# Kernel optimization log

Measured on AMD Instinct MI355X. Metric: run time of the kernel, lower is better.

The kernel has to match this reference:

```python
import jax, jax.numpy as jnp
import numpy as np

EMBED_DIM = 1024
NUM_HEADS = 16
HEAD_DIM = EMBED_DIM // NUM_HEADS
SEG_LENS = [2048, 2048, 4096]
DIL_RATES = [1, 2, 4]
SCALE = 1.0 / np.sqrt(HEAD_DIM)


def _hilbert_perm(L):
    """1D permutation ordering indices of a length-L segment along a Hilbert curve
    on the smallest 2^k x 2^k grid with >= L cells (row-major linearization)."""
    n = 1
    while n * n < L:
        n *= 2
    d = np.arange(n * n)
    x = np.zeros_like(d)
    y = np.zeros_like(d)
    t = d.copy()
    s = 1
    while s < n:
        rx = 1 & (t // 2)
        ry = 1 & (t ^ rx)
        swap = ry == 0
        xr = np.where(swap & (rx == 1), s - 1 - x, x)
        yr = np.where(swap & (rx == 1), s - 1 - y, y)
        x = np.where(swap, yr, xr) + s * rx
        y = np.where(swap, xr, yr) + s * ry
        t = t // 4
        s *= 2
    lin = y * n + x          # linear index visited at each Hilbert distance
    perm = lin[lin < L]      # restrict to valid segment positions
    return np.asarray(perm, dtype=np.int64)

# static per-segment Hilbert permutations and their inverses
_PERMS = [_hilbert_perm(L) for L in SEG_LENS]
_INV_PERMS = [np.argsort(p) for p in _PERMS]


def setup_inputs() -> dict:
    key = jax.random.key(0)
    ks = jax.random.split(key, 5)
    B, S, E = 1, 8192, EMBED_DIM
    x = jax.random.normal(ks[0], (B, S, E), dtype=jnp.float32)
    Wqkv = jax.random.normal(ks[1], (3 * E, E), dtype=jnp.float32) * 0.02
    bqkv = jax.random.normal(ks[2], (3 * E,), dtype=jnp.float32) * 0.02
    Wout = jax.random.normal(ks[3], (E, E), dtype=jnp.float32) * 0.02
    bout = jax.random.normal(ks[4], (E,), dtype=jnp.float32) * 0.02
    return {"x": x, "Wqkv": Wqkv, "bqkv": bqkv, "Wout": Wout, "bout": bout}


def _segment_attention(q, k, v, dil_rate, perm, inv_perm):
    # Hilbert reorder of q/k/v within the segment
    if q.shape[2] > 1:
        q = q[:, :, perm]
        k = k[:, :, perm]
        v = v[:, :, perm]
    # dilation: stride-r subsampling of keys/values (in Hilbert order)
    k_d = k[:, :, ::dil_rate]
    v_d = v[:, :, ::dil_rate]
    scores = jnp.einsum('bhqd,bhkd->bhqk', q, k_d) * SCALE
    out = jnp.einsum('bhqk,bhkd->bhqd', jax.nn.softmax(scores, axis=-1), v_d)
    # reverse Hilbert reorder on the output
    if out.shape[2] > 1:
        out = out[:, :, inv_perm]
    return out


def reference(x, Wqkv, bqkv, Wout, bout):
    B, S, E = x.shape
    H, D = NUM_HEADS, HEAD_DIM
    qkv = x @ Wqkv.T + bqkv                                # [B,S,3E]
    qkv = qkv.reshape(B, S, 3, H, D).transpose(2, 0, 3, 1, 4)  # [3,B,H,S,D]
    q, k, v = qkv[0], qkv[1], qkv[2]
    # disjoint contiguous segment slabs covering the sequence
    outs = []
    pos = 0
    for seg_len, dil, perm, inv in zip(SEG_LENS, DIL_RATES, _PERMS, _INV_PERMS):
        sl = slice(pos, pos + seg_len)
        outs.append(_segment_attention(q[:, :, sl], k[:, :, sl], v[:, :, sl], dil, perm, inv))
        pos += seg_len
    out_h = jnp.concatenate(outs, axis=2)                  # [B,H,S,D]
    out = out_h.transpose(0, 2, 1, 3).reshape(B, S, E)
    return out @ Wout.T + bout
```

## Files before the change

kernel.cpp:

```cpp
#include <hip/hip_runtime.h>
#include <math.h>

typedef short short8 __attribute__((ext_vector_type(8)));
typedef float fx4 __attribute__((ext_vector_type(4)));
typedef unsigned short ushort;
typedef unsigned int uint;
typedef uint uint2v __attribute__((ext_vector_type(2)));

#define MFMA16(a, b, c) __builtin_amdgcn_mfma_f32_16x16x32_bf16(a, b, c, 0, 0, 0)

#define QSCALE 0.180336880f

#define BAR() do { asm volatile("" ::: "memory"); __builtin_amdgcn_s_barrier(); asm volatile("" ::: "memory"); } while (0)
#define VMCNT(n) asm volatile("s_waitcnt vmcnt(" #n ")" ::: "memory")

__device__ __forceinline__ ushort f2bf(float f) {
    union { float f; uint u; } v; v.f = f;
    uint r = v.u + 0x7fffu + ((v.u >> 16) & 1u);
    return (ushort)(r >> 16);
}

__device__ __forceinline__ float exp2f_fast(float x) {
    float r; asm("v_exp_f32 %0, %1" : "=v"(r) : "v"(x)); return r;
}

__device__ __forceinline__ uint cvt_pk_bf16(float lo, float hi) {
    uint r; asm("v_cvt_pk_bf16_f32 %0, %1, %2" : "=v"(r) : "v"(lo), "v"(hi)); return r;
}

__device__ __forceinline__ void gl_lds16(const void* g, void* l) {
    __builtin_amdgcn_global_load_lds(
        (const __attribute__((address_space(1))) void*)g,
        (__attribute__((address_space(3))) void*)l, 16, 0, 0);
}

__device__ ushort g_XB[8192 * 1024];
__device__ ushort g_WQB[3072 * 1024];
__device__ ushort g_WOB[1024 * 1024];
__device__ ushort g_QSEG[16 * 8192 * 64];
__device__ ushort g_KSEG[16 * 4096 * 64];
__device__ ushort g_VSEG[16 * 4096 * 64];
__device__ ushort g_VT[16 * 64 * 4096];
__device__ ushort g_ATTN[8192 * 1024];
__device__ int g_QROW[8192];
__device__ int g_KVROW[8192];
__device__ int g_KVSRC[4096];

__global__ __launch_bounds__(256) void cvt_kernel(const float* __restrict__ x,
                                                  const float* __restrict__ wq,
                                                  const float* __restrict__ wo) {
    int idx = blockIdx.x * 256 + threadIdx.x;
    const int NX = 8192 * 1024 / 4, NQ = 3072 * 1024 / 4, NO = 1024 * 1024 / 4;
    const float* s; ushort* d; int rel;
    if (idx < NX)            { s = x;  d = g_XB;  rel = idx; }
    else if (idx < NX + NQ)  { s = wq; d = g_WQB; rel = idx - NX; }
    else if (idx < NX + NQ + NO) { s = wo; d = g_WOB; rel = idx - NX - NQ; }
    else return;
    fx4 v = *(const fx4*)(s + (long)rel * 4);
    uint lo = f2bf(v[0]) | ((uint)f2bf(v[1]) << 16);
    uint hi = f2bf(v[2]) | ((uint)f2bf(v[3]) << 16);
    uint2v w; w[0] = lo; w[1] = hi;
    *(uint2v*)(d + (long)rel * 4) = w;
}

__global__ __launch_bounds__(1024) void perm_kernel() {
    __shared__ int perm_lds[4096];
    __shared__ int inv_lds[4096];
    __shared__ int sc[1024];
    int seg = blockIdx.x;
    int L     = (seg == 2) ? 4096 : 2048;
    int dil   = (seg == 0) ? 1 : (seg == 1) ? 2 : 4;
    int pos   = (seg == 0) ? 0 : (seg == 1) ? 2048 : 4096;
    int kbase = (seg == 0) ? 0 : (seg == 1) ? 2048 : 3072;
    int tid = threadIdx.x;

    int lin[4]; int flg[4]; int cnt = 0;
    #pragma unroll
    for (int c = 0; c < 4; c++) {
        int d = tid * 4 + c;
        int x = 0, y = 0, t = d;
        for (int s = 1; s < 64; s <<= 1) {
            int rx = (t >> 1) & 1;
            int ry = (t ^ rx) & 1;
            if (ry == 0) {
                if (rx == 1) { x = s - 1 - x; y = s - 1 - y; }
                int tmp = x; x = y; y = tmp;
            }
            x += s * rx; y += s * ry; t >>= 2;
        }
        lin[c] = y * 64 + x;
        flg[c] = (lin[c] < L) ? 1 : 0;
        cnt += flg[c];
    }
    sc[tid] = cnt; __syncthreads();
    for (int off = 1; off < 1024; off <<= 1) {
        int v = sc[tid];
        int a = (tid >= off) ? sc[tid - off] : 0;
        __syncthreads();
        sc[tid] = v + a;
        __syncthreads();
    }
    int base = sc[tid] - cnt;
    #pragma unroll
    for (int c = 0; c < 4; c++) if (flg[c]) perm_lds[base++] = lin[c];
    __syncthreads();
    for (int i = tid; i < L; i += 1024) inv_lds[perm_lds[i]] = i;
    __syncthreads();
    for (int p = tid; p < L; p += 1024) {
        int i = inv_lds[p];
        int s = pos + p;
        g_QROW[s] = pos + i;
        if ((i & (dil - 1)) == 0) {
            int kr = kbase + i / dil;
            g_KVROW[s] = kr;
            g_KVSRC[kr] = s;
        } else {
            g_KVROW[s] = -1;
        }
    }
}


#define GEMM_DEFS                                                             \
    const int tid = threadIdx.x;                                              \
    const int lane = tid & 63;                                                \
    const int wid = tid >> 6;                                                 \
    const int lq = lane & 15, lg = lane >> 4;                                 \
    const int swz = lq & 7;                                                   \
    const int wr = wid >> 2, wc = wid & 3;

#define LD_A(cur)                                                             \
    _Pragma("unroll")                                                         \
    for (int mi = 0; mi < 4; mi++)                                            \
        _Pragma("unroll")                                                     \
        for (int kk = 0; kk < 2; kk++)                                        \
            af[mi][kk] = *(const short8*)(&AT[cur][(wr * 64 + mi * 16 + lq) * 64 + (((kk * 4 + lg) ^ swz) << 3)]);
#define LD_B0(cur)                                                            \
    _Pragma("unroll")                                                         \
    for (int nj = 0; nj < 2; nj++)                                            \
        _Pragma("unroll")                                                     \
        for (int kk = 0; kk < 2; kk++)                                        \
            bf0[nj][kk] = *(const short8*)(&BT[cur][(wc * 32 + nj * 16 + lq) * 64 + (((kk * 4 + lg) ^ swz) << 3)]);
#define LD_B1(cur)                                                            \
    _Pragma("unroll")                                                         \
    for (int nj = 0; nj < 2; nj++)                                            \
        _Pragma("unroll")                                                     \
        for (int kk = 0; kk < 2; kk++)                                        \
            bf1[nj][kk] = *(const short8*)(&BT[cur][(128 + wc * 32 + nj * 16 + lq) * 64 + (((kk * 4 + lg) ^ swz) << 3)]);
#define MM0()                                                                 \
    __builtin_amdgcn_s_setprio(1);                                            \
    _Pragma("unroll")                                                         \
    for (int kk = 0; kk < 2; kk++)                                            \
        _Pragma("unroll")                                                     \
        for (int mi = 0; mi < 4; mi++)                                        \
            _Pragma("unroll")                                                 \
            for (int nj = 0; nj < 2; nj++)                                    \
                acc[mi][nj] = MFMA16(af[mi][kk], bf0[nj][kk], acc[mi][nj]);    \
    __builtin_amdgcn_s_setprio(0);
#define MM1()                                                                 \
    __builtin_amdgcn_s_setprio(1);                                            \
    _Pragma("unroll")                                                         \
    for (int kk = 0; kk < 2; kk++)                                            \
        _Pragma("unroll")                                                     \
        for (int mi = 0; mi < 4; mi++)                                        \
            _Pragma("unroll")                                                 \
            for (int nj = 0; nj < 2; nj++)                                    \
                acc[mi][nj + 2] = MFMA16(af[mi][kk], bf1[nj][kk], acc[mi][nj + 2]); \
    __builtin_amdgcn_s_setprio(0);

#define STG_A(b, kt_) do { gl_lds16(sA0 + (kt_) * 64, &AT[b][ca0 * 8]);      \
                           gl_lds16(sA1 + (kt_) * 64, &AT[b][ca1 * 8]); } while (0)
#define STG_B0(b, kt_) do { gl_lds16(sB[0] + (kt_) * 64, &BT[b][tid * 8]);   \
                            gl_lds16(sB[1] + (kt_) * 64, &BT[b][(tid + 512) * 8]); } while (0)
#define STG_B1(b, kt_) do { gl_lds16(sB[2] + (kt_) * 64, &BT[b][(tid + 1024) * 8]); \
                            gl_lds16(sB[3] + (kt_) * 64, &BT[b][(tid + 1536) * 8]); } while (0)

#define GEMM_MAIN_LOOP                                                        \
    STG_A(0, 0); STG_B0(0, 0); STG_B1(0, 0);                                  \
    VMCNT(2);                                                                 \
    BAR();                                                                    \
    for (int kt = 0; kt < 15; kt++) {                                         \
        int cur = kt & 1, nxt = cur ^ 1;                                      \
        LD_A(cur); LD_B0(cur);                                                \
        STG_A(nxt, kt + 1); STG_B0(nxt, kt + 1);                              \
        MM0();                                                                \
        VMCNT(4);                                                             \
        BAR();                                                                \
        LD_B1(cur);                                                           \
        STG_B1(nxt, kt + 1);                                                  \
        MM1();                                                                \
        VMCNT(2);                                                             \
        BAR();                                                                \
    }                                                                         \
    LD_A(1); LD_B0(1);                                                        \
    MM0();                                                                    \
    VMCNT(0);                                                                 \
    BAR();                                                                    \
    LD_B1(1);                                                                 \
    MM1();

__global__ __launch_bounds__(512, 2) void qkv_q(const float* __restrict__ bias) {
    __shared__ __align__(16) ushort AT[2][128 * 64];
    __shared__ __align__(16) ushort BT[2][256 * 64];
    GEMM_DEFS
    const int row0 = blockIdx.x * 128, col0 = blockIdx.y * 256;

    int ca0 = tid, ca1 = tid + 512;
    int ra0 = ca0 >> 3, pa0 = (ca0 & 7) ^ (ra0 & 7);
    int ra1 = ca1 >> 3, pa1 = (ca1 & 7) ^ (ra1 & 7);
    const ushort* sA0 = g_XB + (long)(row0 + ra0) * 1024 + pa0 * 8;
    const ushort* sA1 = g_XB + (long)(row0 + ra1) * 1024 + pa1 * 8;
    const ushort* sB[4];
    #pragma unroll
    for (int j = 0; j < 4; j++) {
        int c = tid + 512 * j;
        int r = c >> 3, p = (c & 7) ^ (r & 7);
        sB[j] = g_WQB + (long)(col0 + r) * 1024 + p * 8;
    }

    fx4 acc[4][4] = {};
    short8 af[4][2], bf0[2][2], bf1[2][2];

    GEMM_MAIN_LOOP

    #pragma unroll
    for (int mi = 0; mi < 4; mi++)
        #pragma unroll
        for (int r = 0; r < 4; r++) {
            int m = row0 + wr * 64 + mi * 16 + lg * 4 + r;
            int qr = g_QROW[m];
            #pragma unroll
            for (int nj = 0; nj < 4; nj++) {
                int n = col0 + (nj >> 1) * 128 + wc * 32 + (nj & 1) * 16 + lq;
                float val = acc[mi][nj][r] + bias[n];
                int h = n >> 6, dd = n & 63;
                g_QSEG[((long)h * 8192 + qr) * 64 + dd] = f2bf(val * QSCALE);
            }
        }
}

__global__ __launch_bounds__(512, 2) void qkv_kv(const float* __restrict__ bias) {
    __shared__ __align__(16) ushort AT[2][128 * 64];
    __shared__ __align__(16) ushort BT[2][256 * 64];
    GEMM_DEFS
    const int row0 = blockIdx.x * 128, col0 = blockIdx.y * 256;

    int ca0 = tid, ca1 = tid + 512;
    int ra0 = ca0 >> 3, pa0 = (ca0 & 7) ^ (ra0 & 7);
    int ra1 = ca1 >> 3, pa1 = (ca1 & 7) ^ (ra1 & 7);
    const ushort* sA0 = g_XB + (long)g_KVSRC[row0 + ra0] * 1024 + pa0 * 8;
    const ushort* sA1 = g_XB + (long)g_KVSRC[row0 + ra1] * 1024 + pa1 * 8;
    const ushort* sB[4];
    #pragma unroll
    for (int j = 0; j < 4; j++) {
        int c = tid + 512 * j;
        int r = c >> 3, p = (c & 7) ^ (r & 7);
        sB[j] = g_WQB + (long)(1024 + col0 + r) * 1024 + p * 8;
    }

    fx4 acc[4][4] = {};
    short8 af[4][2], bf0[2][2], bf1[2][2];

    GEMM_MAIN_LOOP

    #pragma unroll
    for (int mi = 0; mi < 4; mi++)
        #pragma unroll
        for (int r = 0; r < 4; r++) {
            int m = row0 + wr * 64 + mi * 16 + lg * 4 + r;
            #pragma unroll
            for (int nj = 0; nj < 4; nj++) {
                int n = col0 + (nj >> 1) * 128 + wc * 32 + (nj & 1) * 16 + lq;
                float val = acc[mi][nj][r] + bias[1024 + n];
                int h = (n >> 6) & 15, dd = n & 63;
                if (n < 1024) g_KSEG[((long)h * 4096 + m) * 64 + dd] = f2bf(val);
                else          g_VSEG[((long)h * 4096 + m) * 64 + dd] = f2bf(val);
            }
        }
}

__global__ __launch_bounds__(512, 2) void out_gemm8(const float* __restrict__ bias,
                                                    float* __restrict__ out) {
    __shared__ __align__(16) ushort AT[2][128 * 64];
    __shared__ __align__(16) ushort BT[2][256 * 64];
    GEMM_DEFS
    const int row0 = blockIdx.x * 128, col0 = blockIdx.y * 256;

    int ca0 = tid, ca1 = tid + 512;
    int ra0 = ca0 >> 3, pa0 = (ca0 & 7) ^ (ra0 & 7);
    int ra1 = ca1 >> 3, pa1 = (ca1 & 7) ^ (ra1 & 7);
    const ushort* sA0 = g_ATTN + (long)g_QROW[row0 + ra0] * 1024 + pa0 * 8;
    const ushort* sA1 = g_ATTN + (long)g_QROW[row0 + ra1] * 1024 + pa1 * 8;
    const ushort* sB[4];
    #pragma unroll
    for (int j = 0; j < 4; j++) {
        int c = tid + 512 * j;
        int r = c >> 3, p = (c & 7) ^ (r & 7);
        sB[j] = g_WOB + (long)(col0 + r) * 1024 + p * 8;
    }

    fx4 acc[4][4] = {};
    short8 af[4][2], bf0[2][2], bf1[2][2];

    GEMM_MAIN_LOOP

    #pragma unroll
    for (int mi = 0; mi < 4; mi++)
        #pragma unroll
        for (int r = 0; r < 4; r++) {
            int mm = row0 + wr * 64 + mi * 16 + lg * 4 + r;
            #pragma unroll
            for (int nj = 0; nj < 4; nj++) {
                int n = col0 + (nj >> 1) * 128 + wc * 32 + (nj & 1) * 16 + lq;
                out[(long)mm * 1024 + n] = acc[mi][nj][r] + bias[n];
            }
        }
}

__global__ __launch_bounds__(256) void vtrans_kernel() {
    __shared__ __align__(16) ushort tile[64 * 80];
    int b = blockIdx.x; int h = b >> 6; int rt = b & 63;
    const ushort* src = g_VSEG + ((long)h * 4096 + rt * 64) * 64;
    int tid = threadIdx.x;
    for (int c = tid; c < 512; c += 256) {
        int row = c >> 3, ch = c & 7;
        *(short8*)&tile[row * 80 + ch * 8] = *(const short8*)(src + row * 64 + ch * 8);
    }
    __syncthreads();
    for (int c = tid; c < 512; c += 256) {
        int d = c >> 3, oc = c & 7;
        ushort tmp[8];
        #pragma unroll
        for (int e = 0; e < 8; e++) tmp[e] = tile[(oc * 8 + e) * 80 + d];
        *(short8*)&g_VT[((long)h * 64 + d) * 4096 + rt * 64 + oc * 8] = *(short8*)tmp;
    }
}

__global__ __launch_bounds__(256, 3) void attn_kernel() {
    __shared__ __align__(16) ushort Kt[2][64 * 64];
    __shared__ __align__(16) ushort Vt[2][64 * 64];
    __shared__ __align__(16) ushort Plds[4][32 * 72];
    int bid = blockIdx.x;
    int seg, h, qblk;
    if (bid < 256)      { seg = 0; h = bid >> 4;         qblk = bid & 15; }
    else if (bid < 512) { seg = 1; h = (bid - 256) >> 4; qblk = (bid - 256) & 15; }
    else                { seg = 2; h = (bid - 512) >> 5; qblk = (bid - 512) & 31; }
    int qbase = (seg == 0) ? 0 : (seg == 1) ? 2048 : 4096;
    int kbase = (seg == 0) ? 0 : (seg == 1) ? 2048 : 3072;
    int nkt   = (seg == 0) ? 32 : 16;

    int tid = threadIdx.x;
    int lane = tid & 63, wid = tid >> 6;
    int lq = lane & 15, lg = lane >> 4;
    int swz = lq & 7;
    int qrow0 = qbase + qblk * 128 + wid * 32;

    const ushort* kseg = g_KSEG + (long)h * 4096 * 64;
    const ushort* vtb0 = g_VT + (long)h * 64 * 4096 + kbase;
    ushort* P = &Plds[wid][0];

    int c0 = tid, c1 = tid + 256;
    int r0 = c0 >> 3, e0 = (c0 & 7) ^ (r0 & 7);
    int r1 = c1 >> 3, e1 = (c1 & 7) ^ (r1 & 7);
    const ushort* ka0 = kseg + (long)(kbase + r0) * 64 + e0 * 8;
    const ushort* ka1 = kseg + (long)(kbase + r1) * 64 + e1 * 8;
    const ushort* va0 = vtb0 + (long)r0 * 4096 + e0 * 8;
    const ushort* va1 = vtb0 + (long)r1 * 4096 + e1 * 8;

#define STAGE(b, kt_) do {                                                    \
        gl_lds16(ka0 + (long)(kt_) * 4096, &Kt[b][c0 * 8]);                   \
        gl_lds16(ka1 + (long)(kt_) * 4096, &Kt[b][c1 * 8]);                   \
        gl_lds16(va0 + (kt_) * 64, &Vt[b][c0 * 8]);                           \
        gl_lds16(va1 + (kt_) * 64, &Vt[b][c1 * 8]);                           \
    } while (0)

    const ushort* qp = g_QSEG + ((long)h * 8192 + qrow0) * 64;
    short8 qf[2][2];
    #pragma unroll
    for (int qt = 0; qt < 2; qt++)
        #pragma unroll
        for (int hf = 0; hf < 2; hf++)
            qf[qt][hf] = *(const short8*)(qp + (qt * 16 + lq) * 64 + hf * 32 + lg * 8);

    short8 onesA;
    #pragma unroll
    for (int i = 0; i < 8; i++) onesA[i] = (short)0x3F80;

    STAGE(0, 0);
    asm volatile("s_waitcnt vmcnt(0)" ::: "memory");
    __syncthreads();

    fx4 accT[4][2] = {};
    fx4 lacc[2] = {};
    float m0 = -INFINITY, m1 = -INFINITY;

#define BODY(cur, kt_) do {                                                   \
        if ((kt_) + 1 < nkt) STAGE((cur) ^ 1, (kt_) + 1);                     \
        const ushort* Kc = Kt[cur];                                           \
        const ushort* Vc = Vt[cur];                                           \
        short8 kf[4][2];                                                      \
        _Pragma("unroll")                                                     \
        for (int t = 0; t < 4; t++)                                           \
            _Pragma("unroll")                                                 \
            for (int hf = 0; hf < 2; hf++)                                    \
                kf[t][hf] = *(const short8*)(Kc + (t * 16 + lq) * 64 + (((hf * 4 + lg) ^ swz) << 3)); \
        fx4 st[4][2];                                                         \
        __builtin_amdgcn_s_setprio(1);                                        \
        _Pragma("unroll")                                                     \
        for (int t = 0; t < 4; t++)                                           \
            _Pragma("unroll")                                                 \
            for (int qt = 0; qt < 2; qt++) {                                  \
                fx4 s = {};                                                   \
                s = MFMA16(kf[t][0], qf[qt][0], s);                           \
                s = MFMA16(kf[t][1], qf[qt][1], s);                           \
                st[t][qt] = s;                                                \
            }                                                                 \
        __builtin_amdgcn_s_setprio(0);                                        \
        float t0, t1;                                                         \
        {                                                                     \
            fx4 mx0 = st[0][0], mx1 = st[0][1];                               \
            _Pragma("unroll")                                                 \
            for (int t = 1; t < 4; t++) {                                     \
                mx0 = fx4{fmaxf(mx0[0], st[t][0][0]), fmaxf(mx0[1], st[t][0][1]), \
                          fmaxf(mx0[2], st[t][0][2]), fmaxf(mx0[3], st[t][0][3])}; \
                mx1 = fx4{fmaxf(mx1[0], st[t][1][0]), fmaxf(mx1[1], st[t][1][1]), \
                          fmaxf(mx1[2], st[t][1][2]), fmaxf(mx1[3], st[t][1][3])}; \
            }                                                                 \
            t0 = fmaxf(fmaxf(mx0[0], mx0[1]), fmaxf(mx0[2], mx0[3]));         \
            t1 = fmaxf(fmaxf(mx1[0], mx1[1]), fmaxf(mx1[2], mx1[3]));         \
            t0 = fmaxf(t0, __shfl_xor(t0, 16)); t0 = fmaxf(t0, __shfl_xor(t0, 32)); \
            t1 = fmaxf(t1, __shfl_xor(t1, 16)); t1 = fmaxf(t1, __shfl_xor(t1, 32)); \
        }                                                                     \
        if (__any((t0 > m0 + 8.f) || (t1 > m1 + 8.f))) {                      \
            float nm0 = fmaxf(m0, t0), nm1 = fmaxf(m1, t1);                   \
            float cr0 = exp2f_fast(m0 - nm0), cr1 = exp2f_fast(m1 - nm1);     \
            m0 = nm0; m1 = nm1;                                               \
            lacc[0] *= cr0; lacc[1] *= cr1;                                   \
            _Pragma("unroll")                                                 \
            for (int td = 0; td < 4; td++) {                                  \
                accT[td][0] *= cr0;                                           \
                accT[td][1] *= cr1;                                           \
            }                                                                 \
        }                                                                     \
        _Pragma("unroll")                                                     \
        for (int qt = 0; qt < 2; qt++) {                                      \
            float mm = qt ? m1 : m0;                                          \
            _Pragma("unroll")                                                 \
            for (int t = 0; t < 4; t++) {                                     \
                float p0 = exp2f_fast(st[t][qt][0] - mm);                     \
                float p1 = exp2f_fast(st[t][qt][1] - mm);                     \
                float p2 = exp2f_fast(st[t][qt][2] - mm);                     \
                float p3 = exp2f_fast(st[t][qt][3] - mm);                     \
                uint2v w;                                                     \
                w[0] = cvt_pk_bf16(p0, p1);                                   \
                w[1] = cvt_pk_bf16(p2, p3);                                   \
                *(uint2v*)(P + (qt * 16 + lq) * 72 + t * 16 + lg * 4) = w;    \
            }                                                                 \
        }                                                                     \
        short8 vf[4][2];                                                      \
        _Pragma("unroll")                                                     \
        for (int td = 0; td < 4; td++)                                        \
            _Pragma("unroll")                                                 \
            for (int hf = 0; hf < 2; hf++)                                    \
                vf[td][hf] = *(const short8*)(Vc + (td * 16 + lq) * 64 + (((hf * 4 + lg) ^ swz) << 3)); \
        __builtin_amdgcn_s_setprio(1);                                        \
        _Pragma("unroll")                                                     \
        for (int qt = 0; qt < 2; qt++) {                                      \
            short8 pb0 = *(const short8*)(P + (qt * 16 + lq) * 72 + lg * 8);  \
            short8 pb1 = *(const short8*)(P + (qt * 16 + lq) * 72 + 32 + lg * 8); \
            lacc[qt] = MFMA16(onesA, pb0, lacc[qt]);                          \
            lacc[qt] = MFMA16(onesA, pb1, lacc[qt]);                          \
            _Pragma("unroll")                                                 \
            for (int td = 0; td < 4; td++) {                                  \
                accT[td][qt] = MFMA16(vf[td][0], pb0, accT[td][qt]);          \
                accT[td][qt] = MFMA16(vf[td][1], pb1, accT[td][qt]);          \
            }                                                                 \
        }                                                                     \
        __builtin_amdgcn_s_setprio(0);                                        \
        asm volatile("s_waitcnt vmcnt(0)" ::: "memory");                      \
        __syncthreads();                                                      \
    } while (0)

    for (int kt = 0; kt < nkt; kt += 2) {
        BODY(0, kt);
        BODY(1, kt + 1);
    }
#undef BODY
#undef STAGE

    float ri0 = 1.0f / lacc[0][0];
    float ri1 = 1.0f / lacc[1][0];
    #pragma unroll
    for (int qt = 0; qt < 2; qt++) {
        float ri = qt ? ri1 : ri0;
        ushort* op = g_ATTN + (long)(qrow0 + qt * 16 + lq) * 1024 + h * 64;
        #pragma unroll
        for (int td = 0; td < 4; td++) {
            uint2v w;
            w[0] = cvt_pk_bf16(accT[td][qt][0] * ri, accT[td][qt][1] * ri);
            w[1] = cvt_pk_bf16(accT[td][qt][2] * ri, accT[td][qt][3] * ri);
            *(uint2v*)(op + td * 16 + lg * 4) = w;
        }
    }
}

extern "C" void kernel_launch(void* const* d_in, const int* in_sizes, int n_in,
                              void* d_out, int out_size, void* d_ws, size_t ws_size,
                              hipStream_t stream) {
    const float* x    = (const float*)d_in[0];
    const float* Wqkv = (const float*)d_in[1];
    const float* bqkv = (const float*)d_in[2];
    const float* Wout = (const float*)d_in[3];
    const float* bout = (const float*)d_in[4];
    float* out = (float*)d_out;
    (void)d_ws; (void)ws_size; (void)in_sizes; (void)n_in; (void)out_size;

    cvt_kernel<<<dim3(12288), dim3(256), 0, stream>>>(x, Wqkv, Wout);
    perm_kernel<<<dim3(3), dim3(1024), 0, stream>>>();
    qkv_q<<<dim3(64, 4), dim3(512), 0, stream>>>(bqkv);
    qkv_kv<<<dim3(32, 8), dim3(512), 0, stream>>>(bqkv);
    vtrans_kernel<<<dim3(1024), dim3(256), 0, stream>>>();
    attn_kernel<<<dim3(1024), dim3(256), 0, stream>>>();
    out_gemm8<<<dim3(64, 4), dim3(512), 0, stream>>>(bout, out);
}
```

Measured before the change: 163.4 us.

## Rewrite attention kernel with 32x32 MFMA and register-resident P via permlane32 swap

The attention inner loop now uses 32x32x16 bf16 MFMAs in place of 16x16x32, computing S transposed so each lane holds a full column of scores. The softmax probabilities stay in registers and are rearranged with permlane32_swap, which removes the per-wave P round trip through LDS and its 16 KB of shared memory. The row sum is accumulated with scalar adds plus one cross-half shuffle instead of MFMAs against a ones vector. Launch bounds are raised to 4 blocks per CU to use the freed LDS, at the cost of more register pressure and a different output store pattern.

```diff
diff --git a/kernel.cpp b/kernel.cpp
--- a/kernel.cpp
+++ b/kernel.cpp
@@ -3,11 +3,13 @@
 
 typedef short short8 __attribute__((ext_vector_type(8)));
 typedef float fx4 __attribute__((ext_vector_type(4)));
+typedef float fx16 __attribute__((ext_vector_type(16)));
 typedef unsigned short ushort;
 typedef unsigned int uint;
 typedef uint uint2v __attribute__((ext_vector_type(2)));
 
 #define MFMA16(a, b, c) __builtin_amdgcn_mfma_f32_16x16x32_bf16(a, b, c, 0, 0, 0)
+#define MFMA32(a, b, c) __builtin_amdgcn_mfma_f32_32x32x16_bf16(a, b, c, 0, 0, 0)
 
 #define QSCALE 0.180336880f
 
@@ -26,6 +28,10 @@
 
 __device__ __forceinline__ uint cvt_pk_bf16(float lo, float hi) {
     uint r; asm("v_cvt_pk_bf16_f32 %0, %1, %2" : "=v"(r) : "v"(lo), "v"(hi)); return r;
+}
+
+__device__ __forceinline__ short8 mk8(uint a, uint b, uint c, uint d) {
+    union { uint u[4]; short8 s; } x; x.u[0] = a; x.u[1] = b; x.u[2] = c; x.u[3] = d; return x.s;
 }
 
 __device__ __forceinline__ void gl_lds16(const void* g, void* l) {
@@ -336,10 +342,9 @@
     }
 }
 
-__global__ __launch_bounds__(256, 3) void attn_kernel() {
+__global__ __launch_bounds__(256, 4) void attn_kernel() {
     __shared__ __align__(16) ushort Kt[2][64 * 64];
     __shared__ __align__(16) ushort Vt[2][64 * 64];
-    __shared__ __align__(16) ushort Plds[4][32 * 72];
     int bid = blockIdx.x;
     int seg, h, qblk;
     if (bid < 256)      { seg = 0; h = bid >> 4;         qblk = bid & 15; }
@@ -351,13 +356,12 @@
 
     int tid = threadIdx.x;
     int lane = tid & 63, wid = tid >> 6;
-    int lq = lane & 15, lg = lane >> 4;
-    int swz = lq & 7;
+    int l5 = lane & 31, hi = lane >> 5;
+    int sw7 = l5 & 7;
     int qrow0 = qbase + qblk * 128 + wid * 32;
 
     const ushort* kseg = g_KSEG + (long)h * 4096 * 64;
     const ushort* vtb0 = g_VT + (long)h * 64 * 4096 + kbase;
-    ushort* P = &Plds[wid][0];
 
     int c0 = tid, c1 = tid + 256;
     int r0 = c0 >> 3, e0 = (c0 & 7) ^ (r0 & 7);
@@ -374,133 +378,109 @@
         gl_lds16(va1 + (kt_) * 64, &Vt[b][c1 * 8]);                           \
     } while (0)
 
-    const ushort* qp = g_QSEG + ((long)h * 8192 + qrow0) * 64;
-    short8 qf[2][2];
-    #pragma unroll
-    for (int qt = 0; qt < 2; qt++)
-        #pragma unroll
-        for (int hf = 0; hf < 2; hf++)
-            qf[qt][hf] = *(const short8*)(qp + (qt * 16 + lq) * 64 + hf * 32 + lg * 8);
-
-    short8 onesA;
-    #pragma unroll
-    for (int i = 0; i < 8; i++) onesA[i] = (short)0x3F80;
+    const ushort* qp = g_QSEG + ((long)h * 8192 + qrow0 + l5) * 64;
+    short8 qf[4];
+    #pragma unroll
+    for (int dc = 0; dc < 4; dc++)
+        qf[dc] = *(const short8*)(qp + dc * 16 + hi * 8);
 
     STAGE(0, 0);
-    asm volatile("s_waitcnt vmcnt(0)" ::: "memory");
+    VMCNT(0);
     __syncthreads();
 
-    fx4 accT[4][2] = {};
-    fx4 lacc[2] = {};
-    float m0 = -INFINITY, m1 = -INFINITY;
-
-#define BODY(cur, kt_) do {                                                   \
-        if ((kt_) + 1 < nkt) STAGE((cur) ^ 1, (kt_) + 1);                     \
-        const ushort* Kc = Kt[cur];                                           \
-        const ushort* Vc = Vt[cur];                                           \
-        short8 kf[4][2];                                                      \
-        _Pragma("unroll")                                                     \
-        for (int t = 0; t < 4; t++)                                           \
-            _Pragma("unroll")                                                 \
-            for (int hf = 0; hf < 2; hf++)                                    \
-                kf[t][hf] = *(const short8*)(Kc + (t * 16 + lq) * 64 + (((hf * 4 + lg) ^ swz) << 3)); \
-        fx4 st[4][2];                                                         \
-        __builtin_amdgcn_s_setprio(1);                                        \
-        _Pragma("unroll")                                                     \
-        for (int t = 0; t < 4; t++)                                           \
-            _Pragma("unroll")                                                 \
-            for (int qt = 0; qt < 2; qt++) {                                  \
-                fx4 s = {};                                                   \
-                s = MFMA16(kf[t][0], qf[qt][0], s);                           \
-                s = MFMA16(kf[t][1], qf[qt][1], s);                           \
-                st[t][qt] = s;                                                \
-            }                                                                 \
-        __builtin_amdgcn_s_setprio(0);                                        \
-        float t0, t1;                                                         \
-        {                                                                     \
-            fx4 mx0 = st[0][0], mx1 = st[0][1];                               \
-            _Pragma("unroll")                                                 \
-            for (int t = 1; t < 4; t++) {                                     \
-                mx0 = fx4{fmaxf(mx0[0], st[t][0][0]), fmaxf(mx0[1], st[t][0][1]), \
-                          fmaxf(mx0[2], st[t][0][2]), fmaxf(mx0[3], st[t][0][3])}; \
-                mx1 = fx4{fmaxf(mx1[0], st[t][1][0]), fmaxf(mx1[1], st[t][1][1]), \
-                          fmaxf(mx1[2], st[t][1][2]), fmaxf(mx1[3], st[t][1][3])}; \
-            }                                                                 \
-            t0 = fmaxf(fmaxf(mx0[0], mx0[1]), fmaxf(mx0[2], mx0[3]));         \
-            t1 = fmaxf(fmaxf(mx1[0], mx1[1]), fmaxf(mx1[2], mx1[3]));         \
-            t0 = fmaxf(t0, __shfl_xor(t0, 16)); t0 = fmaxf(t0, __shfl_xor(t0, 32)); \
-            t1 = fmaxf(t1, __shfl_xor(t1, 16)); t1 = fmaxf(t1, __shfl_xor(t1, 32)); \
-        }                                                                     \
-        if (__any((t0 > m0 + 8.f) || (t1 > m1 + 8.f))) {                      \
-            float nm0 = fmaxf(m0, t0), nm1 = fmaxf(m1, t1);                   \
-            float cr0 = exp2f_fast(m0 - nm0), cr1 = exp2f_fast(m1 - nm1);     \
-            m0 = nm0; m1 = nm1;                                               \
-            lacc[0] *= cr0; lacc[1] *= cr1;                                   \
-            _Pragma("unroll")                                                 \
-            for (int td = 0; td < 4; td++) {                                  \
-                accT[td][0] *= cr0;                                           \
-                accT[td][1] *= cr1;                                           \
-            }                                                                 \
-        }                                                                     \
-        _Pragma("unroll")                                                     \
-        for (int qt = 0; qt < 2; qt++) {                                      \
-            float mm = qt ? m1 : m0;                                          \
-            _Pragma("unroll")                                                 \
-            for (int t = 0; t < 4; t++) {                                     \
-                float p0 = exp2f_fast(st[t][qt][0] - mm);                     \
-                float p1 = exp2f_fast(st[t][qt][1] - mm);                     \
-                float p2 = exp2f_fast(st[t][qt][2] - mm);                     \
-                float p3 = exp2f_fast(st[t][qt][3] - mm);                     \
-                uint2v w;                                                     \
-                w[0] = cvt_pk_bf16(p0, p1);                                   \
-                w[1] = cvt_pk_bf16(p2, p3);                                   \
-                *(uint2v*)(P + (qt * 16 + lq) * 72 + t * 16 + lg * 4) = w;    \
-            }                                                                 \
-        }                                                                     \
-        short8 vf[4][2];                                                      \
-        _Pragma("unroll")                                                     \
-        for (int td = 0; td < 4; td++)                                        \
-            _Pragma("unroll")                                                 \
-            for (int hf = 0; hf < 2; hf++)                                    \
-                vf[td][hf] = *(const short8*)(Vc + (td * 16 + lq) * 64 + (((hf * 4 + lg) ^ swz) << 3)); \
-        __builtin_amdgcn_s_setprio(1);                                        \
-        _Pragma("unroll")                                                     \
-        for (int qt = 0; qt < 2; qt++) {                                      \
-            short8 pb0 = *(const short8*)(P + (qt * 16 + lq) * 72 + lg * 8);  \
-            short8 pb1 = *(const short8*)(P + (qt * 16 + lq) * 72 + 32 + lg * 8); \
-            lacc[qt] = MFMA16(onesA, pb0, lacc[qt]);                          \
-            lacc[qt] = MFMA16(onesA, pb1, lacc[qt]);                          \
-            _Pragma("unroll")                                                 \
-            for (int td = 0; td < 4; td++) {                                  \
-                accT[td][qt] = MFMA16(vf[td][0], pb0, accT[td][qt]);          \
-                accT[td][qt] = MFMA16(vf[td][1], pb1, accT[td][qt]);          \
-            }                                                                 \
-        }                                                                     \
-        __builtin_amdgcn_s_setprio(0);                                        \
-        asm volatile("s_waitcnt vmcnt(0)" ::: "memory");                      \
-        __syncthreads();                                                      \
-    } while (0)
-
-    for (int kt = 0; kt < nkt; kt += 2) {
-        BODY(0, kt);
-        BODY(1, kt + 1);
-    }
-#undef BODY
+    fx16 accO0 = {}, accO1 = {};
+    float lown = 0.f, m = -INFINITY;
+
+    for (int kt = 0; kt < nkt; kt++) {
+        int cur = kt & 1;
+        if (kt + 1 < nkt) STAGE(cur ^ 1, kt + 1);
+        const ushort* Kc = Kt[cur];
+        const ushort* Vc = Vt[cur];
+
+        fx16 s0 = {}, s1 = {};
+        __builtin_amdgcn_s_setprio(1);
+        #pragma unroll
+        for (int dc = 0; dc < 4; dc++) {
+            short8 kf0 = *(const short8*)(Kc + l5 * 64 + (((2 * dc + hi) ^ sw7) << 3));
+            short8 kf1 = *(const short8*)(Kc + (32 + l5) * 64 + (((2 * dc + hi) ^ sw7) << 3));
+            s0 = MFMA32(kf0, qf[dc], s0);
+            s1 = MFMA32(kf1, qf[dc], s1);
+        }
+        __builtin_amdgcn_s_setprio(0);
+
+        float tm;
+        {
+            fx16 mx;
+            #pragma unroll
+            for (int r = 0; r < 16; r++) mx[r] = fmaxf(s0[r], s1[r]);
+            float t8[8];
+            #pragma unroll
+            for (int r = 0; r < 8; r++) t8[r] = fmaxf(mx[r], mx[r + 8]);
+            float t4a = fmaxf(t8[0], t8[4]), t4b = fmaxf(t8[1], t8[5]);
+            float t4c = fmaxf(t8[2], t8[6]), t4d = fmaxf(t8[3], t8[7]);
+            tm = fmaxf(fmaxf(t4a, t4b), fmaxf(t4c, t4d));
+        }
+        tm = fmaxf(tm, __shfl_xor(tm, 32));
+        if (__any(tm > m + 8.f)) {
+            float nm = fmaxf(m, tm);
+            float cr = exp2f_fast(m - nm);
+            m = nm;
+            lown *= cr;
+            accO0 *= cr;
+            accO1 *= cr;
+        }
+
+        uint dw0[8], dw1[8];
+        float ls = 0.f;
+        #pragma unroll
+        for (int i = 0; i < 8; i++) {
+            float p0 = exp2f_fast(s0[2 * i] - m);
+            float p1 = exp2f_fast(s0[2 * i + 1] - m);
+            float p2 = exp2f_fast(s1[2 * i] - m);
+            float p3 = exp2f_fast(s1[2 * i + 1] - m);
+            ls += (p0 + p1) + (p2 + p3);
+            dw0[i] = cvt_pk_bf16(p0, p1);
+            dw1[i] = cvt_pk_bf16(p2, p3);
+        }
+        lown += ls;
+
+        short8 pb[4];
+        #pragma unroll
+        for (int m4 = 0; m4 < 4; m4++) {
+            int i0 = (m4 & 1) * 4;
+            uint a0 = (m4 >> 1) ? dw1[i0] : dw0[i0];
+            uint a1 = (m4 >> 1) ? dw1[i0 + 1] : dw0[i0 + 1];
+            uint b0 = (m4 >> 1) ? dw1[i0 + 2] : dw0[i0 + 2];
+            uint b1 = (m4 >> 1) ? dw1[i0 + 3] : dw0[i0 + 3];
+            uint2v ra = __builtin_amdgcn_permlane32_swap(a0, b0, false, false);
+            uint2v rb = __builtin_amdgcn_permlane32_swap(a1, b1, false, false);
+            pb[m4] = mk8(ra[0], rb[0], ra[1], rb[1]);
+        }
+
+        __builtin_amdgcn_s_setprio(1);
+        #pragma unroll
+        for (int m4 = 0; m4 < 4; m4++) {
+            short8 vf0 = *(const short8*)(Vc + l5 * 64 + (((2 * m4 + hi) ^ sw7) << 3));
+            short8 vf1 = *(const short8*)(Vc + (32 + l5) * 64 + (((2 * m4 + hi) ^ sw7) << 3));
+            accO0 = MFMA32(vf0, pb[m4], accO0);
+            accO1 = MFMA32(vf1, pb[m4], accO1);
+        }
+        __builtin_amdgcn_s_setprio(0);
+
+        VMCNT(0);
+        __syncthreads();
+    }
 #undef STAGE
 
-    float ri0 = 1.0f / lacc[0][0];
-    float ri1 = 1.0f / lacc[1][0];
-    #pragma unroll
-    for (int qt = 0; qt < 2; qt++) {
-        float ri = qt ? ri1 : ri0;
-        ushort* op = g_ATTN + (long)(qrow0 + qt * 16 + lq) * 1024 + h * 64;
-        #pragma unroll
-        for (int td = 0; td < 4; td++) {
-            uint2v w;
-            w[0] = cvt_pk_bf16(accT[td][qt][0] * ri, accT[td][qt][1] * ri);
-            w[1] = cvt_pk_bf16(accT[td][qt][2] * ri, accT[td][qt][3] * ri);
-            *(uint2v*)(op + td * 16 + lg * 4) = w;
-        }
+    float ri = 1.0f / (lown + __shfl_xor(lown, 32));
+    ushort* op = g_ATTN + (long)(qrow0 + l5) * 1024 + h * 64;
+    #pragma unroll
+    for (int i = 0; i < 8; i++) {
+        uint w0 = cvt_pk_bf16(accO0[2 * i] * ri, accO0[2 * i + 1] * ri);
+        uint w1 = cvt_pk_bf16(accO1[2 * i] * ri, accO1[2 * i + 1] * ri);
+        int d0 = 2 * (i & 1) + 8 * (i >> 1) + 4 * hi;
+        *(uint*)(op + d0) = w0;
+        *(uint*)(op + 32 + d0) = w1;
     }
 }
 
```

New measurement: 161.2 us. No clear change (-1.3%).
